# Kernel optimization log

Measured on AMD Instinct MI355X. Metric: run time of the kernel, lower is better.

The kernel has to match this reference:

```python
import jax, jax.numpy as jnp
import numpy as np

N_NODES = 100000
N_EDGES = 3200000
N_FEAT = 512
HIDDEN = 16
N_CLASSES = 64


def setup_inputs() -> dict:
    key = jax.random.key(0)
    k1, k2, k3, k4 = jax.random.split(key, 4)
    x = jax.random.normal(k1, (N_NODES, N_FEAT), dtype=jnp.float32)
    edge_index = jax.random.randint(k2, (2, N_EDGES), 0, N_NODES, dtype=jnp.int64)
    # Glorot-ish scaling keeps log_softmax numerically tame
    W1 = jax.random.normal(k3, (N_FEAT, HIDDEN), dtype=jnp.float32) / np.sqrt(N_FEAT)
    b1 = jnp.zeros((HIDDEN,), dtype=jnp.float32)
    W2 = jax.random.normal(k4, (HIDDEN, N_CLASSES), dtype=jnp.float32) / np.sqrt(HIDDEN)
    b2 = jnp.zeros((N_CLASSES,), dtype=jnp.float32)
    return {"x": x, "edge_index": edge_index, "W1": W1, "b1": b1, "W2": W2, "b2": b2}


def _gcn_conv(h, src, dst, norm, W, b, num_nodes):
    # dense transform first (PyG GCNConv order), then normalized scatter-add
    h = h @ W                                   # [N, out]
    msg = h[src] * norm[:, None]                # gather + edge scaling [E, out]
    agg = jax.ops.segment_sum(msg, dst, num_segments=num_nodes)
    return agg + b


def reference(x, edge_index, W1, b1, W2, b2):
    N = x.shape[0]
    loop = jnp.arange(N, dtype=edge_index.dtype)
    src = jnp.concatenate([edge_index[0], loop])  # add self-loops
    dst = jnp.concatenate([edge_index[1], loop])
    deg = jax.ops.segment_sum(jnp.ones_like(src, dtype=x.dtype), dst, num_segments=N)
    dinv = jax.lax.rsqrt(jnp.maximum(deg, 1.0))
    norm = dinv[src] * dinv[dst]                  # symmetric D^-1/2 A_hat D^-1/2

    h = jax.nn.relu(_gcn_conv(x, src, dst, norm, W1, b1, N))
    # dropout: identity in eval mode (training=False)
    h = _gcn_conv(h, src, dst, norm, W2, b2, N)
    return jax.nn.log_softmax(h, axis=1)
```

## Files before the change

kernel.cpp:

```cpp
#include <hip/hip_runtime.h>

#define NNODES 100000
#define NEDGES 3200000
#define NFEAT  512
#define NHID   16
#define NCLS   64
#define NB     391
#define CAP    10240
#define EPB    8192

typedef short bf16x8 __attribute__((ext_vector_type(8)));
typedef float f32x4  __attribute__((ext_vector_type(4)));

__device__ __forceinline__ short f2bf(float f) {
    unsigned u = __float_as_uint(f);
    return (short)((u + 0x7FFFu + ((u >> 16) & 1u)) >> 16);
}
__device__ __forceinline__ float bf2f(unsigned short u) {
    return __uint_as_float((unsigned)u << 16);
}

__global__ __launch_bounds__(512) void k_part(const int* __restrict__ src,
                                              const int* __restrict__ dst,
                                              unsigned* __restrict__ gcnt,
                                              unsigned* __restrict__ part) {
    __shared__ unsigned hist[NB];
    __shared__ unsigned scn[512];
    __shared__ unsigned cursor[NB];
    __shared__ unsigned delta[NB];
    __shared__ unsigned staged[EPB];
    __shared__ unsigned short pbkt[EPB];
    int t = threadIdx.x;
    int base = blockIdx.x * EPB;
    int nblk = min(EPB, NEDGES - base);
    for (int i = t; i < NB; i += 512) hist[i] = 0;
    __syncthreads();
    unsigned pk[16]; unsigned short bk[16];
#pragma unroll
    for (int j = 0; j < 16; ++j) {
        int o = t + j * 512;
        if (o < nblk) {
            int s = src[base + o], d = dst[base + o];
            pk[j] = (unsigned)s | ((unsigned)(d & 255) << 17);
            bk[j] = (unsigned short)(d >> 8);
            atomicAdd(&hist[bk[j]], 1u);
        } else bk[j] = 0xFFFFu;
    }
    __syncthreads();
    scn[t] = (t < NB) ? hist[t] : 0u;
    __syncthreads();
#pragma unroll
    for (int off = 1; off < 512; off <<= 1) {
        unsigned a = (t >= off) ? scn[t - off] : 0u;
        __syncthreads();
        scn[t] += a;
        __syncthreads();
    }
    for (int i = t; i < NB; i += 512) {
        unsigned h = hist[i];
        unsigned ex = scn[i] - h;
        cursor[i] = ex;
        unsigned gb = h ? atomicAdd(&gcnt[i], h) : 0u;
        delta[i] = (unsigned)i * CAP + gb - ex;
    }
    __syncthreads();
#pragma unroll
    for (int j = 0; j < 16; ++j) {
        if (bk[j] != 0xFFFFu) {
            unsigned p = atomicAdd(&cursor[bk[j]], 1u);
            staged[p] = pk[j];
            pbkt[p] = bk[j];
        }
    }
    __syncthreads();
    for (int i = t; i < nblk; i += 512) {
        unsigned b = pbkt[i];
        unsigned d = delta[b] + (unsigned)i;
        if (d < (b + 1u) * CAP) part[d] = staged[i];
    }
}

__global__ __launch_bounds__(512) void k_csr(const unsigned* __restrict__ gcnt,
                                             unsigned* __restrict__ part,
                                             unsigned* __restrict__ offs,
                                             unsigned* __restrict__ cnt,
                                             float* __restrict__ dinv) {
    __shared__ unsigned hist[256], nst[256], cursor[256];
    __shared__ unsigned staged[CAP];
    int t = threadIdx.x, b = blockIdx.x;
    unsigned cb = min(gcnt[b], (unsigned)CAP);
    unsigned* seg = part + (size_t)b * CAP;
    if (t < 256) hist[t] = 0;
    __syncthreads();
    for (unsigned i = t; i < cb; i += 512)
        atomicAdd(&hist[(seg[i] >> 17) & 255u], 1u);
    __syncthreads();
    if (t < 256) nst[t] = hist[t];
    __syncthreads();
#pragma unroll
    for (int off = 1; off < 256; off <<= 1) {
        unsigned a = (t >= off && t < 256) ? nst[t - off] : 0u;
        __syncthreads();
        if (t < 256) nst[t] += a;
        __syncthreads();
    }
    if (t < 256) {
        unsigned ex = nst[t] - hist[t];
        cursor[t] = ex;
        int node = b * 256 + t;
        if (node < NNODES) {
            offs[node] = (unsigned)b * CAP + ex;
            cnt[node] = hist[t];
            dinv[node] = rsqrtf((float)hist[t] + 1.f);
        }
    }
    __syncthreads();
    for (unsigned i = t; i < cb; i += 512) {
        unsigned p = seg[i];
        unsigned r = atomicAdd(&cursor[(p >> 17) & 255u], 1u);
        staged[r] = p & 0x1FFFFu;
    }
    __syncthreads();
    for (unsigned i = t; i < cb; i += 512)
        seg[i] = staged[i];
}

__global__ __launch_bounds__(256) void k_gemm1(const float* __restrict__ x,
                                               const float* __restrict__ w1,
                                               const float* __restrict__ dinv,
                                               unsigned short* __restrict__ hs1) {
    __shared__ short w1t[16][520];
    int tid = threadIdx.x;
    for (int idx = tid; idx < NFEAT * NHID; idx += 256) {
        int k = idx >> 4, n = idx & 15;
        w1t[n][k] = f2bf(w1[idx]);
    }
    __syncthreads();
    int wave = tid >> 6, lane = tid & 63;
    int tile = blockIdx.x * 4 + wave;
    if (tile >= NNODES / 16) return;
    int m = lane & 15, q = lane >> 4;
    const float* xrow = x + (size_t)(tile * 16 + m) * NFEAT + q * 8;
    const short* wrow = &w1t[m][q * 8];
    f32x4 acc = {0.f, 0.f, 0.f, 0.f};
#pragma unroll
    for (int kb = 0; kb < NFEAT / 32; ++kb) {
        float4 a0 = *(const float4*)(xrow + kb * 32);
        float4 a1 = *(const float4*)(xrow + kb * 32 + 4);
        bf16x8 a;
        a[0] = f2bf(a0.x); a[1] = f2bf(a0.y); a[2] = f2bf(a0.z); a[3] = f2bf(a0.w);
        a[4] = f2bf(a1.x); a[5] = f2bf(a1.y); a[6] = f2bf(a1.z); a[7] = f2bf(a1.w);
        bf16x8 b = *(const bf16x8*)(wrow + kb * 32);
        acc = __builtin_amdgcn_mfma_f32_16x16x32_bf16(a, b, acc, 0, 0, 0);
    }
    unsigned short* out = hs1 + (size_t)(tile * 16) * NHID;
#pragma unroll
    for (int r = 0; r < 4; ++r) {
        int row = q * 4 + r;
        out[row * NHID + m] = (unsigned short)f2bf(acc[r] * dinv[tile * 16 + row]);
    }
}

__global__ __launch_bounds__(256) void k_agg1(const unsigned* __restrict__ offs,
                                              const unsigned* __restrict__ cnt,
                                              const unsigned* __restrict__ eb,
                                              const unsigned short* __restrict__ hs1,
                                              const float* __restrict__ dinv,
                                              const float* __restrict__ b1,
                                              unsigned short* __restrict__ hs2) {
    int tid = threadIdx.x;
    int node = blockIdx.x * 4 + (tid >> 6);
    int lane = tid & 63, f = lane & 15, slot = lane >> 4;
    unsigned start = offs[node];
    int deg = (int)cnt[node];
    float di = dinv[node];
    float acc = 0.f;
    int rounds = (deg + 31) >> 5;
    int cl = deg - 1;
    for (int r = 0; r < rounds; ++r) {
        int jb = r * 32 + slot * 8;
        unsigned e[8];
#pragma unroll
        for (int u = 0; u < 8; ++u) e[u] = eb[start + min(jb + u, cl)];
        float a[8];
#pragma unroll
        for (int u = 0; u < 8; ++u) a[u] = bf2f(hs1[(size_t)e[u] * NHID + f]);
#pragma unroll
        for (int u = 0; u < 8; ++u) acc += (jb + u < deg) ? a[u] : 0.f;
    }
    acc += __shfl_xor(acc, 16);
    acc += __shfl_xor(acc, 32);
    float v = (acc + bf2f(hs1[(size_t)node * NHID + f])) * di + b1[f];
    v = v > 0.f ? v : 0.f;
    if (slot == 0) hs2[(size_t)node * NHID + f] = (unsigned short)f2bf(v * di);
}

__global__ __launch_bounds__(256) void k_out2(const unsigned* __restrict__ offs,
                                              const unsigned* __restrict__ cnt,
                                              const unsigned* __restrict__ eb,
                                              const unsigned short* __restrict__ hs2,
                                              const float* __restrict__ dinv,
                                              const float* __restrict__ w2,
                                              const float* __restrict__ b2,
                                              float* __restrict__ out) {
    int tid = threadIdx.x;
    int node = blockIdx.x * 4 + (tid >> 6);
    int lane = tid & 63, f = lane & 15, slot = lane >> 4;
    unsigned start = offs[node];
    int deg = (int)cnt[node];
    float di = dinv[node];
    float w2c[NHID];
#pragma unroll
    for (int k = 0; k < NHID; ++k) w2c[k] = w2[k * NCLS + lane];
    float bb = b2[lane];
    float acc = 0.f;
    int rounds = (deg + 31) >> 5;
    int cl = deg - 1;
    for (int r = 0; r < rounds; ++r) {
        int jb = r * 32 + slot * 8;
        unsigned e[8];
#pragma unroll
        for (int u = 0; u < 8; ++u) e[u] = eb[start + min(jb + u, cl)];
        float a[8];
#pragma unroll
        for (int u = 0; u < 8; ++u) a[u] = bf2f(hs2[(size_t)e[u] * NHID + f]);
#pragma unroll
        for (int u = 0; u < 8; ++u) acc += (jb + u < deg) ? a[u] : 0.f;
    }
    acc += __shfl_xor(acc, 16);
    acc += __shfl_xor(acc, 32);
    float v = (acc + bf2f(hs2[(size_t)node * NHID + f])) * di;
    float logit = bb;
#pragma unroll
    for (int k = 0; k < NHID; ++k)
        logit += __shfl(v, k) * w2c[k];
    float mx = logit;
#pragma unroll
    for (int off = 32; off > 0; off >>= 1) mx = fmaxf(mx, __shfl_xor(mx, off));
    float ex = __expf(logit - mx);
    float s = ex;
#pragma unroll
    for (int off = 32; off > 0; off >>= 1) s += __shfl_xor(s, off);
    out[(size_t)node * NCLS + lane] = logit - mx - logf(s);
}

extern "C" void kernel_launch(void* const* d_in, const int* in_sizes, int n_in,
                              void* d_out, int out_size, void* d_ws, size_t ws_size,
                              hipStream_t stream) {
    const float* x  = (const float*)d_in[0];
    const int*   ei = (const int*)d_in[1];
    const float* w1 = (const float*)d_in[2];
    const float* b1 = (const float*)d_in[3];
    const float* w2 = (const float*)d_in[4];
    const float* b2 = (const float*)d_in[5];
    const int* src = ei;
    const int* dst = ei + NEDGES;

    char* ws = (char*)d_ws;
    unsigned* gcnt = (unsigned*)(ws + 0);
    unsigned* offs = (unsigned*)(ws + 2048);
    unsigned* cnt  = (unsigned*)(ws + 402048);
    float*    dinv = (float*)   (ws + 802048);
    unsigned short* hs1 = (unsigned short*)(ws + 1202048);
    unsigned short* hs2 = (unsigned short*)(ws + 4402048);
    unsigned* part = (unsigned*)(ws + 7602048);

    hipMemsetAsync(gcnt, 0, 2048, stream);
    k_part <<<NB, 512, 0, stream>>>(src, dst, gcnt, part);
    k_csr  <<<NB, 512, 0, stream>>>(gcnt, part, offs, cnt, dinv);
    k_gemm1<<<(NNODES / 16 + 3) / 4, 256, 0, stream>>>(x, w1, dinv, hs1);
    k_agg1 <<<NNODES / 4, 256, 0, stream>>>(offs, cnt, part, hs1, dinv, b1, hs2);
    k_out2 <<<NNODES / 4, 256, 0, stream>>>(offs, cnt, part, hs2, dinv, w2, b2, (float*)d_out);
}
```

Before: 437.6 us.

## Replace per-node CSR gather with bucketed LDS atomic scatter and co-run partition/GEMM

Drops the per-bucket CSR sort. The edge partition pass and the first dense transform now run as two disjoint block ranges of one launch, so the GEMM no longer waits for the graph build. Each aggregation kernel handles one 256-node destination bucket: it streams that bucket's packed edges, gathers source features, and accumulates them with shared-memory float atomics. dinv is applied at gather time instead of being folded into the GEMM output. This removes the CSR sort kernel and the per-node degree-imbalanced loops, but it relies on LDS atomic throughput and leaves only 391 blocks for the aggregation kernels, which may limit parallelism.

```diff
diff --git a/kernel.cpp b/kernel.cpp
--- a/kernel.cpp
+++ b/kernel.cpp
@@ -8,6 +8,8 @@
 #define NB     391
 #define CAP    10240
 #define EPB    8192
+#define GTPB   8
+#define NGB    782
 
 typedef short bf16x8 __attribute__((ext_vector_type(8)));
 typedef float f32x4  __attribute__((ext_vector_type(4)));
@@ -20,228 +22,234 @@
     return __uint_as_float((unsigned)u << 16);
 }
 
-__global__ __launch_bounds__(512) void k_part(const int* __restrict__ src,
-                                              const int* __restrict__ dst,
-                                              unsigned* __restrict__ gcnt,
-                                              unsigned* __restrict__ part) {
-    __shared__ unsigned hist[NB];
-    __shared__ unsigned scn[512];
-    __shared__ unsigned cursor[NB];
-    __shared__ unsigned delta[NB];
-    __shared__ unsigned staged[EPB];
-    __shared__ unsigned short pbkt[EPB];
+struct PartShared {
+    unsigned hist[NB];
+    unsigned scn[512];
+    unsigned cursor[NB];
+    unsigned delta[NB];
+    unsigned staged[EPB];
+    unsigned short pbkt[EPB];
+};
+struct GemmShared {
+    short w1t[16][520];
+};
+union FusedShared { PartShared p; GemmShared g; };
+
+__global__ __launch_bounds__(512) void k_fused1(const int* __restrict__ src,
+                                                const int* __restrict__ dst,
+                                                unsigned* __restrict__ gcnt,
+                                                unsigned* __restrict__ part,
+                                                const float* __restrict__ x,
+                                                const float* __restrict__ w1,
+                                                unsigned short* __restrict__ hs1) {
+    __shared__ FusedShared sh;
     int t = threadIdx.x;
-    int base = blockIdx.x * EPB;
-    int nblk = min(EPB, NEDGES - base);
-    for (int i = t; i < NB; i += 512) hist[i] = 0;
-    __syncthreads();
-    unsigned pk[16]; unsigned short bk[16];
-#pragma unroll
-    for (int j = 0; j < 16; ++j) {
-        int o = t + j * 512;
-        if (o < nblk) {
-            int s = src[base + o], d = dst[base + o];
-            pk[j] = (unsigned)s | ((unsigned)(d & 255) << 17);
-            bk[j] = (unsigned short)(d >> 8);
-            atomicAdd(&hist[bk[j]], 1u);
-        } else bk[j] = 0xFFFFu;
-    }
-    __syncthreads();
-    scn[t] = (t < NB) ? hist[t] : 0u;
-    __syncthreads();
-#pragma unroll
-    for (int off = 1; off < 512; off <<= 1) {
-        unsigned a = (t >= off) ? scn[t - off] : 0u;
-        __syncthreads();
-        scn[t] += a;
-        __syncthreads();
-    }
-    for (int i = t; i < NB; i += 512) {
-        unsigned h = hist[i];
-        unsigned ex = scn[i] - h;
-        cursor[i] = ex;
-        unsigned gb = h ? atomicAdd(&gcnt[i], h) : 0u;
-        delta[i] = (unsigned)i * CAP + gb - ex;
-    }
-    __syncthreads();
-#pragma unroll
-    for (int j = 0; j < 16; ++j) {
-        if (bk[j] != 0xFFFFu) {
-            unsigned p = atomicAdd(&cursor[bk[j]], 1u);
-            staged[p] = pk[j];
-            pbkt[p] = bk[j];
-        }
-    }
-    __syncthreads();
-    for (int i = t; i < nblk; i += 512) {
-        unsigned b = pbkt[i];
-        unsigned d = delta[b] + (unsigned)i;
-        if (d < (b + 1u) * CAP) part[d] = staged[i];
-    }
-}
-
-__global__ __launch_bounds__(512) void k_csr(const unsigned* __restrict__ gcnt,
-                                             unsigned* __restrict__ part,
-                                             unsigned* __restrict__ offs,
-                                             unsigned* __restrict__ cnt,
-                                             float* __restrict__ dinv) {
-    __shared__ unsigned hist[256], nst[256], cursor[256];
-    __shared__ unsigned staged[CAP];
+    if (blockIdx.x < NB) {
+        int base = blockIdx.x * EPB;
+        int nblk = min(EPB, NEDGES - base);
+        for (int i = t; i < NB; i += 512) sh.p.hist[i] = 0;
+        __syncthreads();
+        unsigned pk[16]; unsigned short bk[16];
+#pragma unroll
+        for (int j = 0; j < 16; ++j) {
+            int o = t + j * 512;
+            if (o < nblk) {
+                int s = src[base + o], d = dst[base + o];
+                pk[j] = (unsigned)s | ((unsigned)(d & 255) << 17);
+                bk[j] = (unsigned short)(d >> 8);
+                atomicAdd(&sh.p.hist[bk[j]], 1u);
+            } else bk[j] = 0xFFFFu;
+        }
+        __syncthreads();
+        sh.p.scn[t] = (t < NB) ? sh.p.hist[t] : 0u;
+        __syncthreads();
+#pragma unroll
+        for (int off = 1; off < 512; off <<= 1) {
+            unsigned a = (t >= off) ? sh.p.scn[t - off] : 0u;
+            __syncthreads();
+            sh.p.scn[t] += a;
+            __syncthreads();
+        }
+        for (int i = t; i < NB; i += 512) {
+            unsigned h = sh.p.hist[i];
+            unsigned ex = sh.p.scn[i] - h;
+            sh.p.cursor[i] = ex;
+            unsigned gb = h ? atomicAdd(&gcnt[i], h) : 0u;
+            sh.p.delta[i] = (unsigned)i * CAP + gb - ex;
+        }
+        __syncthreads();
+#pragma unroll
+        for (int j = 0; j < 16; ++j) {
+            if (bk[j] != 0xFFFFu) {
+                unsigned p = atomicAdd(&sh.p.cursor[bk[j]], 1u);
+                sh.p.staged[p] = pk[j];
+                sh.p.pbkt[p] = bk[j];
+            }
+        }
+        __syncthreads();
+        for (int i = t; i < nblk; i += 512) {
+            unsigned b = sh.p.pbkt[i];
+            unsigned d = sh.p.delta[b] + (unsigned)i;
+            if (d < (b + 1u) * CAP) part[d] = sh.p.staged[i];
+        }
+    } else {
+        for (int idx = t; idx < NFEAT * NHID; idx += 512) {
+            int k = idx >> 4, n = idx & 15;
+            sh.g.w1t[n][k] = f2bf(w1[idx]);
+        }
+        __syncthreads();
+        int wave = t >> 6, lane = t & 63;
+        int tile = (int)(blockIdx.x - NB) * GTPB + wave;
+        if (tile >= NNODES / 16) return;
+        int m = lane & 15, q = lane >> 4;
+        const float* xrow = x + (size_t)(tile * 16 + m) * NFEAT + q * 8;
+        const short* wrow = &sh.g.w1t[m][q * 8];
+        f32x4 acc = {0.f, 0.f, 0.f, 0.f};
+#pragma unroll
+        for (int kb = 0; kb < NFEAT / 32; ++kb) {
+            float4 a0 = *(const float4*)(xrow + kb * 32);
+            float4 a1 = *(const float4*)(xrow + kb * 32 + 4);
+            bf16x8 a;
+            a[0] = f2bf(a0.x); a[1] = f2bf(a0.y); a[2] = f2bf(a0.z); a[3] = f2bf(a0.w);
+            a[4] = f2bf(a1.x); a[5] = f2bf(a1.y); a[6] = f2bf(a1.z); a[7] = f2bf(a1.w);
+            bf16x8 b = *(const bf16x8*)(wrow + kb * 32);
+            acc = __builtin_amdgcn_mfma_f32_16x16x32_bf16(a, b, acc, 0, 0, 0);
+        }
+        unsigned short* outp = hs1 + (size_t)(tile * 16) * NHID;
+#pragma unroll
+        for (int r = 0; r < 4; ++r)
+            outp[(q * 4 + r) * NHID + m] = (unsigned short)f2bf(acc[r]);
+    }
+}
+
+__global__ __launch_bounds__(512) void k_dinv(const unsigned* __restrict__ gcnt,
+                                              const unsigned* __restrict__ part,
+                                              float* __restrict__ dinv) {
+    __shared__ unsigned hist[256];
     int t = threadIdx.x, b = blockIdx.x;
     unsigned cb = min(gcnt[b], (unsigned)CAP);
-    unsigned* seg = part + (size_t)b * CAP;
+    const unsigned* seg = part + (size_t)b * CAP;
     if (t < 256) hist[t] = 0;
     __syncthreads();
     for (unsigned i = t; i < cb; i += 512)
         atomicAdd(&hist[(seg[i] >> 17) & 255u], 1u);
     __syncthreads();
-    if (t < 256) nst[t] = hist[t];
-    __syncthreads();
-#pragma unroll
-    for (int off = 1; off < 256; off <<= 1) {
-        unsigned a = (t >= off && t < 256) ? nst[t - off] : 0u;
-        __syncthreads();
-        if (t < 256) nst[t] += a;
-        __syncthreads();
-    }
     if (t < 256) {
-        unsigned ex = nst[t] - hist[t];
-        cursor[t] = ex;
-        int node = b * 256 + t;
-        if (node < NNODES) {
-            offs[node] = (unsigned)b * CAP + ex;
-            cnt[node] = hist[t];
-            dinv[node] = rsqrtf((float)hist[t] + 1.f);
-        }
-    }
-    __syncthreads();
-    for (unsigned i = t; i < cb; i += 512) {
-        unsigned p = seg[i];
-        unsigned r = atomicAdd(&cursor[(p >> 17) & 255u], 1u);
-        staged[r] = p & 0x1FFFFu;
-    }
-    __syncthreads();
-    for (unsigned i = t; i < cb; i += 512)
-        seg[i] = staged[i];
-}
-
-__global__ __launch_bounds__(256) void k_gemm1(const float* __restrict__ x,
-                                               const float* __restrict__ w1,
-                                               const float* __restrict__ dinv,
-                                               unsigned short* __restrict__ hs1) {
-    __shared__ short w1t[16][520];
-    int tid = threadIdx.x;
-    for (int idx = tid; idx < NFEAT * NHID; idx += 256) {
-        int k = idx >> 4, n = idx & 15;
-        w1t[n][k] = f2bf(w1[idx]);
-    }
-    __syncthreads();
-    int wave = tid >> 6, lane = tid & 63;
-    int tile = blockIdx.x * 4 + wave;
-    if (tile >= NNODES / 16) return;
-    int m = lane & 15, q = lane >> 4;
-    const float* xrow = x + (size_t)(tile * 16 + m) * NFEAT + q * 8;
-    const short* wrow = &w1t[m][q * 8];
-    f32x4 acc = {0.f, 0.f, 0.f, 0.f};
-#pragma unroll
-    for (int kb = 0; kb < NFEAT / 32; ++kb) {
-        float4 a0 = *(const float4*)(xrow + kb * 32);
-        float4 a1 = *(const float4*)(xrow + kb * 32 + 4);
-        bf16x8 a;
-        a[0] = f2bf(a0.x); a[1] = f2bf(a0.y); a[2] = f2bf(a0.z); a[3] = f2bf(a0.w);
-        a[4] = f2bf(a1.x); a[5] = f2bf(a1.y); a[6] = f2bf(a1.z); a[7] = f2bf(a1.w);
-        bf16x8 b = *(const bf16x8*)(wrow + kb * 32);
-        acc = __builtin_amdgcn_mfma_f32_16x16x32_bf16(a, b, acc, 0, 0, 0);
-    }
-    unsigned short* out = hs1 + (size_t)(tile * 16) * NHID;
-#pragma unroll
-    for (int r = 0; r < 4; ++r) {
-        int row = q * 4 + r;
-        out[row * NHID + m] = (unsigned short)f2bf(acc[r] * dinv[tile * 16 + row]);
-    }
-}
-
-__global__ __launch_bounds__(256) void k_agg1(const unsigned* __restrict__ offs,
-                                              const unsigned* __restrict__ cnt,
-                                              const unsigned* __restrict__ eb,
-                                              const unsigned short* __restrict__ hs1,
-                                              const float* __restrict__ dinv,
-                                              const float* __restrict__ b1,
-                                              unsigned short* __restrict__ hs2) {
-    int tid = threadIdx.x;
-    int node = blockIdx.x * 4 + (tid >> 6);
-    int lane = tid & 63, f = lane & 15, slot = lane >> 4;
-    unsigned start = offs[node];
-    int deg = (int)cnt[node];
-    float di = dinv[node];
-    float acc = 0.f;
-    int rounds = (deg + 31) >> 5;
-    int cl = deg - 1;
-    for (int r = 0; r < rounds; ++r) {
-        int jb = r * 32 + slot * 8;
-        unsigned e[8];
-#pragma unroll
-        for (int u = 0; u < 8; ++u) e[u] = eb[start + min(jb + u, cl)];
-        float a[8];
-#pragma unroll
-        for (int u = 0; u < 8; ++u) a[u] = bf2f(hs1[(size_t)e[u] * NHID + f]);
-#pragma unroll
-        for (int u = 0; u < 8; ++u) acc += (jb + u < deg) ? a[u] : 0.f;
-    }
-    acc += __shfl_xor(acc, 16);
-    acc += __shfl_xor(acc, 32);
-    float v = (acc + bf2f(hs1[(size_t)node * NHID + f])) * di + b1[f];
-    v = v > 0.f ? v : 0.f;
-    if (slot == 0) hs2[(size_t)node * NHID + f] = (unsigned short)f2bf(v * di);
-}
-
-__global__ __launch_bounds__(256) void k_out2(const unsigned* __restrict__ offs,
-                                              const unsigned* __restrict__ cnt,
-                                              const unsigned* __restrict__ eb,
-                                              const unsigned short* __restrict__ hs2,
-                                              const float* __restrict__ dinv,
-                                              const float* __restrict__ w2,
-                                              const float* __restrict__ b2,
-                                              float* __restrict__ out) {
-    int tid = threadIdx.x;
-    int node = blockIdx.x * 4 + (tid >> 6);
-    int lane = tid & 63, f = lane & 15, slot = lane >> 4;
-    unsigned start = offs[node];
-    int deg = (int)cnt[node];
-    float di = dinv[node];
+        int gn = b * 256 + t;
+        if (gn < NNODES) dinv[gn] = rsqrtf((float)hist[t] + 1.f);
+    }
+}
+
+__global__ __launch_bounds__(512) void k_sc1(const unsigned* __restrict__ gcnt,
+                                             const unsigned* __restrict__ part,
+                                             const float* __restrict__ dinv,
+                                             const unsigned short* __restrict__ hs1,
+                                             const float* __restrict__ b1,
+                                             unsigned short* __restrict__ hs2) {
+    __shared__ float acc[256 * 16];
+    __shared__ unsigned pld[2048];
+    int t = threadIdx.x, b = blockIdx.x;
+    for (int i = t; i < 4096; i += 512) acc[i] = 0.f;
+    unsigned cb = min(gcnt[b], (unsigned)CAP);
+    const unsigned* seg = part + (size_t)b * CAP;
+    int f = t & 15, eslot = t >> 4;
+    for (unsigned chunk = 0; chunk < cb; chunk += 2048) {
+        int n = (int)min(2048u, cb - chunk);
+        for (int i = t; i < n; i += 512) pld[i] = seg[chunk + i];
+        __syncthreads();
+        for (int base = 0; base < n; base += 256) {
+            float m[8]; int nl[8]; bool ok[8];
+#pragma unroll
+            for (int u = 0; u < 8; ++u) {
+                int e = base + u * 32 + eslot;
+                ok[u] = e < n;
+                unsigned p = pld[ok[u] ? e : 0];
+                int s = (int)(p & 0x1FFFFu);
+                nl[u] = (int)((p >> 17) & 255u);
+                float ds = dinv[s];
+                m[u] = bf2f(hs1[(size_t)s * NHID + f]) * ds;
+            }
+#pragma unroll
+            for (int u = 0; u < 8; ++u)
+                if (ok[u]) atomicAdd(&acc[nl[u] * 16 + f], m[u]);
+        }
+        __syncthreads();
+    }
+    for (int i = t; i < 4096; i += 512) {
+        int nd = i >> 4, ff = i & 15;
+        int gn = b * 256 + nd;
+        if (gn < NNODES) {
+            float di = dinv[gn];
+            float v = (acc[i] + bf2f(hs1[(size_t)gn * NHID + ff]) * di) * di + b1[ff];
+            v = v > 0.f ? v : 0.f;
+            hs2[(size_t)gn * NHID + ff] = (unsigned short)f2bf(v * di);
+        }
+    }
+}
+
+__global__ __launch_bounds__(512) void k_sc2(const unsigned* __restrict__ gcnt,
+                                             const unsigned* __restrict__ part,
+                                             const float* __restrict__ dinv,
+                                             const unsigned short* __restrict__ hs2,
+                                             const float* __restrict__ w2,
+                                             const float* __restrict__ b2,
+                                             float* __restrict__ out) {
+    __shared__ float acc[256 * 16];
+    __shared__ unsigned pld[2048];
+    int t = threadIdx.x, b = blockIdx.x;
+    int lane = t & 63, wv = t >> 6;
     float w2c[NHID];
 #pragma unroll
     for (int k = 0; k < NHID; ++k) w2c[k] = w2[k * NCLS + lane];
     float bb = b2[lane];
-    float acc = 0.f;
-    int rounds = (deg + 31) >> 5;
-    int cl = deg - 1;
-    for (int r = 0; r < rounds; ++r) {
-        int jb = r * 32 + slot * 8;
-        unsigned e[8];
-#pragma unroll
-        for (int u = 0; u < 8; ++u) e[u] = eb[start + min(jb + u, cl)];
-        float a[8];
-#pragma unroll
-        for (int u = 0; u < 8; ++u) a[u] = bf2f(hs2[(size_t)e[u] * NHID + f]);
-#pragma unroll
-        for (int u = 0; u < 8; ++u) acc += (jb + u < deg) ? a[u] : 0.f;
-    }
-    acc += __shfl_xor(acc, 16);
-    acc += __shfl_xor(acc, 32);
-    float v = (acc + bf2f(hs2[(size_t)node * NHID + f])) * di;
-    float logit = bb;
-#pragma unroll
-    for (int k = 0; k < NHID; ++k)
-        logit += __shfl(v, k) * w2c[k];
-    float mx = logit;
-#pragma unroll
-    for (int off = 32; off > 0; off >>= 1) mx = fmaxf(mx, __shfl_xor(mx, off));
-    float ex = __expf(logit - mx);
-    float s = ex;
-#pragma unroll
-    for (int off = 32; off > 0; off >>= 1) s += __shfl_xor(s, off);
-    out[(size_t)node * NCLS + lane] = logit - mx - logf(s);
+    for (int i = t; i < 4096; i += 512) acc[i] = 0.f;
+    unsigned cb = min(gcnt[b], (unsigned)CAP);
+    const unsigned* seg = part + (size_t)b * CAP;
+    int f = t & 15, eslot = t >> 4;
+    for (unsigned chunk = 0; chunk < cb; chunk += 2048) {
+        int n = (int)min(2048u, cb - chunk);
+        for (int i = t; i < n; i += 512) pld[i] = seg[chunk + i];
+        __syncthreads();
+        for (int base = 0; base < n; base += 256) {
+            float m[8]; int nl[8]; bool ok[8];
+#pragma unroll
+            for (int u = 0; u < 8; ++u) {
+                int e = base + u * 32 + eslot;
+                ok[u] = e < n;
+                unsigned p = pld[ok[u] ? e : 0];
+                int s = (int)(p & 0x1FFFFu);
+                nl[u] = (int)((p >> 17) & 255u);
+                m[u] = bf2f(hs2[(size_t)s * NHID + f]);
+            }
+#pragma unroll
+            for (int u = 0; u < 8; ++u)
+                if (ok[u]) atomicAdd(&acc[nl[u] * 16 + f], m[u]);
+        }
+        __syncthreads();
+    }
+    for (int i = t; i < 4096; i += 512) {
+        int nd = i >> 4, ff = i & 15;
+        int gn = b * 256 + nd;
+        if (gn < NNODES)
+            acc[i] = (acc[i] + bf2f(hs2[(size_t)gn * NHID + ff])) * dinv[gn];
+    }
+    __syncthreads();
+    for (int nd = wv; nd < 256; nd += 8) {
+        int gn = b * 256 + nd;
+        if (gn >= NNODES) continue;
+        float logit = bb;
+#pragma unroll
+        for (int k = 0; k < NHID; ++k)
+            logit += acc[nd * 16 + k] * w2c[k];
+        float mx = logit;
+#pragma unroll
+        for (int off = 32; off > 0; off >>= 1) mx = fmaxf(mx, __shfl_xor(mx, off));
+        float ex = __expf(logit - mx);
+        float s = ex;
+#pragma unroll
+        for (int off = 32; off > 0; off >>= 1) s += __shfl_xor(s, off);
+        out[(size_t)gn * NCLS + lane] = logit - mx - logf(s);
+    }
 }
 
 extern "C" void kernel_launch(void* const* d_in, const int* in_sizes, int n_in,
@@ -258,17 +266,14 @@
 
     char* ws = (char*)d_ws;
     unsigned* gcnt = (unsigned*)(ws + 0);
-    unsigned* offs = (unsigned*)(ws + 2048);
-    unsigned* cnt  = (unsigned*)(ws + 402048);
-    float*    dinv = (float*)   (ws + 802048);
-    unsigned short* hs1 = (unsigned short*)(ws + 1202048);
-    unsigned short* hs2 = (unsigned short*)(ws + 4402048);
-    unsigned* part = (unsigned*)(ws + 7602048);
+    float*    dinv = (float*)   (ws + 2048);
+    unsigned short* hs1 = (unsigned short*)(ws + 402048);
+    unsigned short* hs2 = (unsigned short*)(ws + 3602048);
+    unsigned* part = (unsigned*)(ws + 6802048);
 
     hipMemsetAsync(gcnt, 0, 2048, stream);
-    k_part <<<NB, 512, 0, stream>>>(src, dst, gcnt, part);
-    k_csr  <<<NB, 512, 0, stream>>>(gcnt, part, offs, cnt, dinv);
-    k_gemm1<<<(NNODES / 16 + 3) / 4, 256, 0, stream>>>(x, w1, dinv, hs1);
-    k_agg1 <<<NNODES / 4, 256, 0, stream>>>(offs, cnt, part, hs1, dinv, b1, hs2);
-    k_out2 <<<NNODES / 4, 256, 0, stream>>>(offs, cnt, part, hs2, dinv, w2, b2, (float*)d_out);
-}
+    k_fused1<<<NB + NGB, 512, 0, stream>>>(src, dst, gcnt, part, x, w1, hs1);
+    k_dinv  <<<NB, 512, 0, stream>>>(gcnt, part, dinv);
+    k_sc1   <<<NB, 512, 0, stream>>>(gcnt, part, dinv, hs1, b1, hs2);
+    k_sc2   <<<NB, 512, 0, stream>>>(gcnt, part, dinv, hs2, w2, b2, (float*)d_out);
+}
```

After: 1.061 ms. 2.42x slower.

## Fuse edge partitioning with dense GEMM in one launch, move dinv scaling into aggregation

Applied to the files above, without the earlier changes.

The edge-partition kernel and the x@W1 GEMM are merged into a single heterogeneous launch, with blocks split by index, so the bandwidth-heavy GEMM overlaps the atomic-heavy partitioning. To remove the GEMM's dependence on dinv, which is computed later by k_csr, the source-degree normalization is moved into the first aggregation as a per-edge dinv gather. The partition block size is halved to give more blocks, and both aggregation loops now process 16 edges per slot per round instead of 8. The extra per-edge dinv gather and the higher register use in aggregation are the costs.

```diff
diff --git a/kernel.cpp b/kernel.cpp
--- a/kernel.cpp
+++ b/kernel.cpp
@@ -7,7 +7,10 @@
 #define NCLS   64
 #define NB     391
 #define CAP    10240
-#define EPB    8192
+#define EPB    4096
+#define NPB    782
+#define GTPB   8
+#define NGB    782
 
 typedef short bf16x8 __attribute__((ext_vector_type(8)));
 typedef float f32x4  __attribute__((ext_vector_type(4)));
@@ -20,63 +23,101 @@
     return __uint_as_float((unsigned)u << 16);
 }
 
-__global__ __launch_bounds__(512) void k_part(const int* __restrict__ src,
-                                              const int* __restrict__ dst,
-                                              unsigned* __restrict__ gcnt,
-                                              unsigned* __restrict__ part) {
-    __shared__ unsigned hist[NB];
-    __shared__ unsigned scn[512];
-    __shared__ unsigned cursor[NB];
-    __shared__ unsigned delta[NB];
-    __shared__ unsigned staged[EPB];
-    __shared__ unsigned short pbkt[EPB];
+struct PartShared {
+    unsigned hist[NB];
+    unsigned scn[512];
+    unsigned cursor[NB];
+    unsigned delta[NB];
+    unsigned staged[EPB];
+    unsigned short pbkt[EPB];
+};
+struct GemmShared { short w1t[16][520]; };
+union FusedShared { PartShared p; GemmShared g; };
+
+__global__ __launch_bounds__(512) void k_fused1(const int* __restrict__ src,
+                                                const int* __restrict__ dst,
+                                                unsigned* __restrict__ gcnt,
+                                                unsigned* __restrict__ part,
+                                                const float* __restrict__ x,
+                                                const float* __restrict__ w1,
+                                                unsigned short* __restrict__ hs1) {
+    __shared__ FusedShared sh;
     int t = threadIdx.x;
-    int base = blockIdx.x * EPB;
-    int nblk = min(EPB, NEDGES - base);
-    for (int i = t; i < NB; i += 512) hist[i] = 0;
-    __syncthreads();
-    unsigned pk[16]; unsigned short bk[16];
-#pragma unroll
-    for (int j = 0; j < 16; ++j) {
-        int o = t + j * 512;
-        if (o < nblk) {
-            int s = src[base + o], d = dst[base + o];
-            pk[j] = (unsigned)s | ((unsigned)(d & 255) << 17);
-            bk[j] = (unsigned short)(d >> 8);
-            atomicAdd(&hist[bk[j]], 1u);
-        } else bk[j] = 0xFFFFu;
-    }
-    __syncthreads();
-    scn[t] = (t < NB) ? hist[t] : 0u;
-    __syncthreads();
-#pragma unroll
-    for (int off = 1; off < 512; off <<= 1) {
-        unsigned a = (t >= off) ? scn[t - off] : 0u;
-        __syncthreads();
-        scn[t] += a;
-        __syncthreads();
-    }
-    for (int i = t; i < NB; i += 512) {
-        unsigned h = hist[i];
-        unsigned ex = scn[i] - h;
-        cursor[i] = ex;
-        unsigned gb = h ? atomicAdd(&gcnt[i], h) : 0u;
-        delta[i] = (unsigned)i * CAP + gb - ex;
-    }
-    __syncthreads();
-#pragma unroll
-    for (int j = 0; j < 16; ++j) {
-        if (bk[j] != 0xFFFFu) {
-            unsigned p = atomicAdd(&cursor[bk[j]], 1u);
-            staged[p] = pk[j];
-            pbkt[p] = bk[j];
-        }
-    }
-    __syncthreads();
-    for (int i = t; i < nblk; i += 512) {
-        unsigned b = pbkt[i];
-        unsigned d = delta[b] + (unsigned)i;
-        if (d < (b + 1u) * CAP) part[d] = staged[i];
+    if (blockIdx.x < NPB) {
+        int base = blockIdx.x * EPB;
+        int nblk = min(EPB, NEDGES - base);
+        for (int i = t; i < NB; i += 512) sh.p.hist[i] = 0;
+        __syncthreads();
+        unsigned pk[8]; unsigned short bk[8];
+#pragma unroll
+        for (int j = 0; j < 8; ++j) {
+            int o = t + j * 512;
+            if (o < nblk) {
+                int s = src[base + o], d = dst[base + o];
+                pk[j] = (unsigned)s | ((unsigned)(d & 255) << 17);
+                bk[j] = (unsigned short)(d >> 8);
+                atomicAdd(&sh.p.hist[bk[j]], 1u);
+            } else bk[j] = 0xFFFFu;
+        }
+        __syncthreads();
+        sh.p.scn[t] = (t < NB) ? sh.p.hist[t] : 0u;
+        __syncthreads();
+#pragma unroll
+        for (int off = 1; off < 512; off <<= 1) {
+            unsigned a = (t >= off) ? sh.p.scn[t - off] : 0u;
+            __syncthreads();
+            sh.p.scn[t] += a;
+            __syncthreads();
+        }
+        for (int i = t; i < NB; i += 512) {
+            unsigned h = sh.p.hist[i];
+            unsigned ex = sh.p.scn[i] - h;
+            sh.p.cursor[i] = ex;
+            unsigned gb = h ? atomicAdd(&gcnt[i], h) : 0u;
+            sh.p.delta[i] = (unsigned)i * CAP + gb - ex;
+        }
+        __syncthreads();
+#pragma unroll
+        for (int j = 0; j < 8; ++j) {
+            if (bk[j] != 0xFFFFu) {
+                unsigned p = atomicAdd(&sh.p.cursor[bk[j]], 1u);
+                sh.p.staged[p] = pk[j];
+                sh.p.pbkt[p] = bk[j];
+            }
+        }
+        __syncthreads();
+        for (int i = t; i < nblk; i += 512) {
+            unsigned b = sh.p.pbkt[i];
+            unsigned d = sh.p.delta[b] + (unsigned)i;
+            if (d < (b + 1u) * CAP) part[d] = sh.p.staged[i];
+        }
+    } else {
+        for (int idx = t; idx < NFEAT * NHID; idx += 512) {
+            int k = idx >> 4, n = idx & 15;
+            sh.g.w1t[n][k] = f2bf(w1[idx]);
+        }
+        __syncthreads();
+        int wave = t >> 6, lane = t & 63;
+        int tile = (int)(blockIdx.x - NPB) * GTPB + wave;
+        if (tile >= NNODES / 16) return;
+        int m = lane & 15, q = lane >> 4;
+        const float* xrow = x + (size_t)(tile * 16 + m) * NFEAT + q * 8;
+        const short* wrow = &sh.g.w1t[m][q * 8];
+        f32x4 acc = {0.f, 0.f, 0.f, 0.f};
+#pragma unroll
+        for (int kb = 0; kb < NFEAT / 32; ++kb) {
+            float4 a0 = *(const float4*)(xrow + kb * 32);
+            float4 a1 = *(const float4*)(xrow + kb * 32 + 4);
+            bf16x8 a;
+            a[0] = f2bf(a0.x); a[1] = f2bf(a0.y); a[2] = f2bf(a0.z); a[3] = f2bf(a0.w);
+            a[4] = f2bf(a1.x); a[5] = f2bf(a1.y); a[6] = f2bf(a1.z); a[7] = f2bf(a1.w);
+            bf16x8 b = *(const bf16x8*)(wrow + kb * 32);
+            acc = __builtin_amdgcn_mfma_f32_16x16x32_bf16(a, b, acc, 0, 0, 0);
+        }
+        unsigned short* outp = hs1 + (size_t)(tile * 16) * NHID;
+#pragma unroll
+        for (int r = 0; r < 4; ++r)
+            outp[(q * 4 + r) * NHID + m] = (unsigned short)f2bf(acc[r]);
     }
 }
 
@@ -123,42 +164,6 @@
     __syncthreads();
     for (unsigned i = t; i < cb; i += 512)
         seg[i] = staged[i];
-}
-
-__global__ __launch_bounds__(256) void k_gemm1(const float* __restrict__ x,
-                                               const float* __restrict__ w1,
-                                               const float* __restrict__ dinv,
-                                               unsigned short* __restrict__ hs1) {
-    __shared__ short w1t[16][520];
-    int tid = threadIdx.x;
-    for (int idx = tid; idx < NFEAT * NHID; idx += 256) {
-        int k = idx >> 4, n = idx & 15;
-        w1t[n][k] = f2bf(w1[idx]);
-    }
-    __syncthreads();
-    int wave = tid >> 6, lane = tid & 63;
-    int tile = blockIdx.x * 4 + wave;
-    if (tile >= NNODES / 16) return;
-    int m = lane & 15, q = lane >> 4;
-    const float* xrow = x + (size_t)(tile * 16 + m) * NFEAT + q * 8;
-    const short* wrow = &w1t[m][q * 8];
-    f32x4 acc = {0.f, 0.f, 0.f, 0.f};
-#pragma unroll
-    for (int kb = 0; kb < NFEAT / 32; ++kb) {
-        float4 a0 = *(const float4*)(xrow + kb * 32);
-        float4 a1 = *(const float4*)(xrow + kb * 32 + 4);
-        bf16x8 a;
-        a[0] = f2bf(a0.x); a[1] = f2bf(a0.y); a[2] = f2bf(a0.z); a[3] = f2bf(a0.w);
-        a[4] = f2bf(a1.x); a[5] = f2bf(a1.y); a[6] = f2bf(a1.z); a[7] = f2bf(a1.w);
-        bf16x8 b = *(const bf16x8*)(wrow + kb * 32);
-        acc = __builtin_amdgcn_mfma_f32_16x16x32_bf16(a, b, acc, 0, 0, 0);
-    }
-    unsigned short* out = hs1 + (size_t)(tile * 16) * NHID;
-#pragma unroll
-    for (int r = 0; r < 4; ++r) {
-        int row = q * 4 + r;
-        out[row * NHID + m] = (unsigned short)f2bf(acc[r] * dinv[tile * 16 + row]);
-    }
 }
 
 __global__ __launch_bounds__(256) void k_agg1(const unsigned* __restrict__ offs,
@@ -175,22 +180,24 @@
     int deg = (int)cnt[node];
     float di = dinv[node];
     float acc = 0.f;
-    int rounds = (deg + 31) >> 5;
+    int rounds = (deg + 63) >> 6;
     int cl = deg - 1;
     for (int r = 0; r < rounds; ++r) {
-        int jb = r * 32 + slot * 8;
-        unsigned e[8];
-#pragma unroll
-        for (int u = 0; u < 8; ++u) e[u] = eb[start + min(jb + u, cl)];
-        float a[8];
-#pragma unroll
-        for (int u = 0; u < 8; ++u) a[u] = bf2f(hs1[(size_t)e[u] * NHID + f]);
-#pragma unroll
-        for (int u = 0; u < 8; ++u) acc += (jb + u < deg) ? a[u] : 0.f;
+        int jb = r * 64 + slot * 16;
+        unsigned e[16];
+#pragma unroll
+        for (int u = 0; u < 16; ++u) e[u] = eb[start + min(jb + u, cl)];
+        float d[16], a[16];
+#pragma unroll
+        for (int u = 0; u < 16; ++u) d[u] = dinv[e[u]];
+#pragma unroll
+        for (int u = 0; u < 16; ++u) a[u] = bf2f(hs1[(size_t)e[u] * NHID + f]);
+#pragma unroll
+        for (int u = 0; u < 16; ++u) acc += (jb + u < deg) ? a[u] * d[u] : 0.f;
     }
     acc += __shfl_xor(acc, 16);
     acc += __shfl_xor(acc, 32);
-    float v = (acc + bf2f(hs1[(size_t)node * NHID + f])) * di + b1[f];
+    float v = (acc + bf2f(hs1[(size_t)node * NHID + f]) * di) * di + b1[f];
     v = v > 0.f ? v : 0.f;
     if (slot == 0) hs2[(size_t)node * NHID + f] = (unsigned short)f2bf(v * di);
 }
@@ -214,18 +221,18 @@
     for (int k = 0; k < NHID; ++k) w2c[k] = w2[k * NCLS + lane];
     float bb = b2[lane];
     float acc = 0.f;
-    int rounds = (deg + 31) >> 5;
+    int rounds = (deg + 63) >> 6;
     int cl = deg - 1;
     for (int r = 0; r < rounds; ++r) {
-        int jb = r * 32 + slot * 8;
-        unsigned e[8];
-#pragma unroll
-        for (int u = 0; u < 8; ++u) e[u] = eb[start + min(jb + u, cl)];
-        float a[8];
-#pragma unroll
-        for (int u = 0; u < 8; ++u) a[u] = bf2f(hs2[(size_t)e[u] * NHID + f]);
-#pragma unroll
-        for (int u = 0; u < 8; ++u) acc += (jb + u < deg) ? a[u] : 0.f;
+        int jb = r * 64 + slot * 16;
+        unsigned e[16];
+#pragma unroll
+        for (int u = 0; u < 16; ++u) e[u] = eb[start + min(jb + u, cl)];
+        float a[16];
+#pragma unroll
+        for (int u = 0; u < 16; ++u) a[u] = bf2f(hs2[(size_t)e[u] * NHID + f]);
+#pragma unroll
+        for (int u = 0; u < 16; ++u) acc += (jb + u < deg) ? a[u] : 0.f;
     }
     acc += __shfl_xor(acc, 16);
     acc += __shfl_xor(acc, 32);
@@ -266,9 +273,8 @@
     unsigned* part = (unsigned*)(ws + 7602048);
 
     hipMemsetAsync(gcnt, 0, 2048, stream);
-    k_part <<<NB, 512, 0, stream>>>(src, dst, gcnt, part);
+    k_fused1<<<NPB + NGB, 512, 0, stream>>>(src, dst, gcnt, part, x, w1, hs1);
     k_csr  <<<NB, 512, 0, stream>>>(gcnt, part, offs, cnt, dinv);
-    k_gemm1<<<(NNODES / 16 + 3) / 4, 256, 0, stream>>>(x, w1, dinv, hs1);
     k_agg1 <<<NNODES / 4, 256, 0, stream>>>(offs, cnt, part, hs1, dinv, b1, hs2);
     k_out2 <<<NNODES / 4, 256, 0, stream>>>(offs, cnt, part, hs2, dinv, w2, b2, (float*)d_out);
 }
```

New measurement: 470.9 us. +7.6%, slower.
